# Kernel tuning notes

Measured on AMD Instinct MI355X. Metric: run time of the kernel, lower is better.

Reference implementation:

```python
import jax, jax.numpy as jnp
import numpy as np
from jax import lax

B, T = 2048, 256
V, E, H = 128, 128, 64
POS_WEIGHT = 20.0


def setup_inputs() -> dict:
    key = jax.random.key(0)
    ks = jax.random.split(key, 9)
    # indices in [1, V) so padding_idx=0 row (zeroed) is unused
    x = jax.random.randint(ks[0], (B, T), 1, V)
    targets = (jax.random.uniform(ks[1], (B,)) < 0.05).astype(jnp.float32)
    emb = jax.random.normal(ks[2], (V, E), dtype=jnp.float32).at[0].set(0.0)  # padding_idx=0
    k = 1.0 / np.sqrt(H)
    W_ih = jax.random.uniform(ks[3], (4 * H, E), minval=-k, maxval=k, dtype=jnp.float32)
    W_hh = jax.random.uniform(ks[4], (4 * H, H), minval=-k, maxval=k, dtype=jnp.float32)
    b_ih = jax.random.uniform(ks[5], (4 * H,), minval=-k, maxval=k, dtype=jnp.float32)
    b_hh = jax.random.uniform(ks[6], (4 * H,), minval=-k, maxval=k, dtype=jnp.float32)
    W_fc = jax.random.uniform(ks[7], (1, H), minval=-k, maxval=k, dtype=jnp.float32)
    b_fc = jax.random.uniform(ks[8], (1,), minval=-k, maxval=k, dtype=jnp.float32)
    return {"x": x, "targets": targets, "emb": emb, "W_ih": W_ih, "W_hh": W_hh,
            "b_ih": b_ih, "b_hh": b_hh, "W_fc": W_fc, "b_fc": b_fc}


def reference(x, targets, emb, W_ih, W_hh, b_ih, b_hh, W_fc, b_fc):
    xe = emb[x]  # [B, T, E]
    # precompute input-to-hidden projections for all timesteps: [B, T, 4H]
    xp = jnp.einsum('bte,ge->btg', xe, W_ih) + b_ih + b_hh
    h0 = jnp.zeros((xe.shape[0], W_hh.shape[1]), dtype=xe.dtype)
    c0 = jnp.zeros_like(h0)

    def step(carry, xt):
        h, c = carry
        gates = xt + h @ W_hh.T  # [B, 4H], PyTorch gate order: i, f, g, o
        i, f, g, o = jnp.split(gates, 4, axis=-1)
        c = jax.nn.sigmoid(f) * c + jax.nn.sigmoid(i) * jnp.tanh(g)
        h = jax.nn.sigmoid(o) * jnp.tanh(c)
        return (h, c), None

    (hT, _), _ = lax.scan(step, (h0, c0), jnp.swapaxes(xp, 0, 1))  # scan over time
    logits = (hT @ W_fc.T + b_fc)[:, 0]  # [B]
    # BCEWithLogits with pos_weight, mean reduction (numerically stable)
    loss = -(POS_WEIGHT * targets * jax.nn.log_sigmoid(logits)
             + (1.0 - targets) * jax.nn.log_sigmoid(-logits)).mean()
    return logits, loss
```

## Files before the change

### kernel.cpp

```cpp
#include <hip/hip_runtime.h>
#include <stdint.h>

#define B_ 2048
#define T_ 256
#define V_ 128
#define E_ 128
#define H_ 64
#define G4_ 256
#define POS_W 20.0f
#define MB_ 8
#define NBLK_ (B_ / MB_)

typedef _Float16 half1;
typedef __attribute__((ext_vector_type(8))) _Float16 f16x8;
typedef __attribute__((ext_vector_type(4))) float f32x4;

#if __has_builtin(__builtin_amdgcn_exp2f)
#define EXP2F(x) __builtin_amdgcn_exp2f(x)
#else
#define EXP2F(x) exp2f(x)
#endif

#if __has_builtin(__builtin_amdgcn_rcpf)
#define RCPF(x) __builtin_amdgcn_rcpf(x)
#else
#define RCPF(x) (1.0f / (x))
#endif

__device__ __forceinline__ float sigm(float x) {
    return RCPF(1.0f + EXP2F(-1.44269504f * x));
}
__device__ __forceinline__ float tanhr(float x) {
    float t = EXP2F(2.88539008f * x);
    return 1.0f - 2.0f * RCPF(t + 1.0f);
}

__device__ __forceinline__ void lds_barrier() {
    asm volatile("s_waitcnt lgkmcnt(0)\n\ts_barrier" ::: "memory");
}

__global__ void k_prep(const float* __restrict__ emb, const float* __restrict__ Wih,
                       const float* __restrict__ bih, const float* __restrict__ bhh,
                       float* __restrict__ projC, float* __restrict__ loss_slot) {
    int tid = threadIdx.x;
    int v = blockIdx.x;
    if (v == 0 && tid == 0) *loss_slot = 0.0f;
    int u = tid >> 2, g = tid & 3;
    int row = g * 64 + u;
    const float4* e4 = (const float4*)(emb + v * E_);
    const float4* w4 = (const float4*)(Wih + row * E_);
    float acc = bih[row] + bhh[row];
#pragma unroll
    for (int i = 0; i < E_ / 4; ++i) {
        float4 a = e4[i];
        float4 b = w4[i];
        acc += a.x * b.x + a.y * b.y + a.z * b.z + a.w * b.w;
    }
    projC[v * G4_ + tid] = acc;
}

__launch_bounds__(256, 1)
__global__ void k_lstm(const int* __restrict__ x, const float* __restrict__ Whh,
                       const float* __restrict__ projC, const float* __restrict__ Wfc,
                       const float* __restrict__ bfc, const float* __restrict__ targets,
                       float* __restrict__ logits, float* __restrict__ loss_slot) {
    int b0 = blockIdx.x * MB_;
    int t = threadIdx.x;
    int w = t >> 6, l = t & 63;
    int q = l >> 4, cc = l & 15;
    int u = 16 * w + cc;
    int rA = 2 * q;

    __shared__ __align__(16) half1 hf[2][1024];
    __shared__ int xT[T_][8];
    __shared__ float hfin[MB_][68];
    __shared__ float zred[MB_];

#pragma unroll
    for (int i = 0; i < MB_; ++i) xT[t][i] = x[(b0 + i) * T_ + t];
    ((float*)hf)[t] = 0.0f;
    ((float*)hf)[t + 256] = 0.0f;
    ((float*)hf)[t + 512] = 0.0f;
    ((float*)hf)[t + 768] = 0.0f;
    __syncthreads();

    f16x8 bf[4][2];
#pragma unroll
    for (int jj = 0; jj < 4; ++jj) {
#pragma unroll
        for (int c = 0; c < 2; ++c) {
            int row = jj * 64 + 16 * w + cc;
            int kb = c * 32 + q * 8;
            float4 w0 = *(const float4*)(Whh + row * H_ + kb);
            float4 w1 = *(const float4*)(Whh + row * H_ + kb + 4);
            f16x8 tmp;
            tmp[0] = (half1)w0.x; tmp[1] = (half1)w0.y;
            tmp[2] = (half1)w0.z; tmp[3] = (half1)w0.w;
            tmp[4] = (half1)w1.x; tmp[5] = (half1)w1.y;
            tmp[6] = (half1)w1.z; tmp[7] = (half1)w1.w;
            bf[jj][c] = tmp;
        }
    }

    int hbase = (u >> 5) * 512 + ((u >> 3) & 3) * 128 + (u & 7) + (4 * q) * 8;

    float cA = 0.0f, cB = 0.0f, hA = 0.0f, hB = 0.0f;

    int2 v0 = *(const int2*)&xT[0][rA];
    int2 v1 = *(const int2*)&xT[1][rA];
    f32x4 ppA = *(const f32x4*)(projC + v0.x * G4_ + u * 4);
    f32x4 ppB = *(const f32x4*)(projC + v0.y * G4_ + u * 4);
    f32x4 pnA = *(const f32x4*)(projC + v1.x * G4_ + u * 4);
    f32x4 pnB = *(const f32x4*)(projC + v1.y * G4_ + u * 4);

    int p = 0;
#pragma unroll 2
    for (int step = 0; step < T_; ++step) {
        int2 v2 = *(const int2*)&xT[(step + 2) & (T_ - 1)][rA];
        f32x4 p2A = *(const f32x4*)(projC + v2.x * G4_ + u * 4);
        f32x4 p2B = *(const f32x4*)(projC + v2.y * G4_ + u * 4);

        const f16x8 a0 = *(const f16x8*)(hf[p] + l * 8);
        const f16x8 a1 = *(const f16x8*)(hf[p] + 512 + l * 8);

        f32x4 z4 = {0.0f, 0.0f, 0.0f, 0.0f};
        float gA[4], gB[4];
#pragma unroll
        for (int jj = 0; jj < 4; ++jj) {
            f32x4 d0 = __builtin_amdgcn_mfma_f32_16x16x32_f16(a0, bf[jj][0], z4, 0, 0, 0);
            f32x4 d1 = __builtin_amdgcn_mfma_f32_16x16x32_f16(a1, bf[jj][1], z4, 0, 0, 0);
            gA[jj] = d0[0] + d1[0];
            gB[jj] = d0[1] + d1[1];
        }

        float iA = sigm(gA[0] + ppA.x);
        float fA = sigm(gA[1] + ppA.y);
        float ggA = tanhr(gA[2] + ppA.z);
        float oA = sigm(gA[3] + ppA.w);
        cA = fA * cA + iA * ggA;
        hA = oA * tanhr(cA);

        float iB = sigm(gB[0] + ppB.x);
        float fB = sigm(gB[1] + ppB.y);
        float ggB = tanhr(gB[2] + ppB.z);
        float oB = sigm(gB[3] + ppB.w);
        cB = fB * cB + iB * ggB;
        hB = oB * tanhr(cB);

        half1* hw = hf[p ^ 1] + hbase;
        hw[0] = (half1)hA;
        hw[8] = (half1)hB;

        ppA = pnA; ppB = pnB;
        pnA = p2A; pnB = p2B;
        p ^= 1;
        lds_barrier();
    }

    hfin[rA][u] = hA;
    hfin[rA + 1][u] = hB;
    __syncthreads();
    int m8 = t >> 5, uu = t & 31;
    float part = hfin[m8][2 * uu] * Wfc[2 * uu] + hfin[m8][2 * uu + 1] * Wfc[2 * uu + 1];
#pragma unroll
    for (int off = 16; off > 0; off >>= 1) part += __shfl_down(part, off, 32);
    if (uu == 0) {
        float z = part + bfc[0];
        logits[b0 + m8] = z;
        float tg = targets[b0 + m8];
        float e = EXP2F(-1.44269504f * fabsf(z));
        float lsp = fminf(z, 0.0f) - log1pf(e);
        float lsn = lsp - z;
        zred[m8] = -(POS_W * tg * lsp + (1.0f - tg) * lsn) * (1.0f / (float)B_);
    }
    __syncthreads();
    if (t == 0) {
        float s = 0.0f;
#pragma unroll
        for (int i = 0; i < MB_; ++i) s += zred[i];
        atomicAdd(loss_slot, s);
    }
}

extern "C" void kernel_launch(void* const* d_in, const int* in_sizes, int n_in,
                              void* d_out, int out_size, void* d_ws, size_t ws_size,
                              hipStream_t stream) {
    const int* x = (const int*)d_in[0];
    const float* targets = (const float*)d_in[1];
    const float* emb = (const float*)d_in[2];
    const float* Wih = (const float*)d_in[3];
    const float* Whh = (const float*)d_in[4];
    const float* bih = (const float*)d_in[5];
    const float* bhh = (const float*)d_in[6];
    const float* Wfc = (const float*)d_in[7];
    const float* bfc = (const float*)d_in[8];
    float* out = (float*)d_out;

    float* projC = (float*)d_ws;

    k_prep<<<dim3(V_), dim3(256), 0, stream>>>(emb, Wih, bih, bhh, projC, out + B_);
    k_lstm<<<dim3(NBLK_), dim3(256), 0, stream>>>(x, Whh, projC, Wfc, bfc, targets, out,
                                                  out + B_);
}
```

Measured before the change: 172.2 us.

## Halve batch rows per LSTM block and run two blocks per CU

```diff
diff --git a/kernel.cpp b/kernel.cpp
--- a/kernel.cpp
+++ b/kernel.cpp
@@ -8,9 +8,8 @@
 #define H_ 64
 #define G4_ 256
 #define POS_W 20.0f
-#define MB_ 8
+#define MB_ 4
 #define NBLK_ (B_ / MB_)
-
 typedef _Float16 half1;
 typedef __attribute__((ext_vector_type(8))) _Float16 f16x8;
 typedef __attribute__((ext_vector_type(4))) float f32x4;
@@ -59,7 +58,7 @@
     projC[v * G4_ + tid] = acc;
 }
 
-__launch_bounds__(256, 1)
+__launch_bounds__(256, 2)
 __global__ void k_lstm(const int* __restrict__ x, const float* __restrict__ Whh,
                        const float* __restrict__ projC, const float* __restrict__ Wfc,
                        const float* __restrict__ bfc, const float* __restrict__ targets,
@@ -69,10 +68,9 @@
     int w = t >> 6, l = t & 63;
     int q = l >> 4, cc = l & 15;
     int u = 16 * w + cc;
-    int rA = 2 * q;
 
     __shared__ __align__(16) half1 hf[2][1024];
-    __shared__ int xT[T_][8];
+    __shared__ int xT[T_][MB_];
     __shared__ float hfin[MB_][68];
     __shared__ float zred[MB_];
 
@@ -102,35 +100,28 @@
         }
     }
 
-    int hbase = (u >> 5) * 512 + ((u >> 3) & 3) * 128 + (u & 7) + (4 * q) * 8;
+    int hbase = (u >> 5) * 512 + ((u >> 3) & 3) * 128 + (4 * q) * 8 + (u & 7);
 
-    float cA = 0.0f, cB = 0.0f, hA = 0.0f, hB = 0.0f;
+    float cA = 0.0f, hA = 0.0f;
 
-    int2 v0 = *(const int2*)&xT[0][rA];
-    int2 v1 = *(const int2*)&xT[1][rA];
-    f32x4 ppA = *(const f32x4*)(projC + v0.x * G4_ + u * 4);
-    f32x4 ppB = *(const f32x4*)(projC + v0.y * G4_ + u * 4);
-    f32x4 pnA = *(const f32x4*)(projC + v1.x * G4_ + u * 4);
-    f32x4 pnB = *(const f32x4*)(projC + v1.y * G4_ + u * 4);
+    f32x4 ppA = *(const f32x4*)(projC + xT[0][q] * G4_ + u * 4);
+    f32x4 pnA = *(const f32x4*)(projC + xT[1][q] * G4_ + u * 4);
 
     int p = 0;
 #pragma unroll 2
     for (int step = 0; step < T_; ++step) {
-        int2 v2 = *(const int2*)&xT[(step + 2) & (T_ - 1)][rA];
-        f32x4 p2A = *(const f32x4*)(projC + v2.x * G4_ + u * 4);
-        f32x4 p2B = *(const f32x4*)(projC + v2.y * G4_ + u * 4);
+        f32x4 p2A = *(const f32x4*)(projC + xT[(step + 2) & (T_ - 1)][q] * G4_ + u * 4);
 
         const f16x8 a0 = *(const f16x8*)(hf[p] + l * 8);
         const f16x8 a1 = *(const f16x8*)(hf[p] + 512 + l * 8);
 
         f32x4 z4 = {0.0f, 0.0f, 0.0f, 0.0f};
-        float gA[4], gB[4];
+        float gA[4];
 #pragma unroll
         for (int jj = 0; jj < 4; ++jj) {
             f32x4 d0 = __builtin_amdgcn_mfma_f32_16x16x32_f16(a0, bf[jj][0], z4, 0, 0, 0);
             f32x4 d1 = __builtin_amdgcn_mfma_f32_16x16x32_f16(a1, bf[jj][1], z4, 0, 0, 0);
             gA[jj] = d0[0] + d1[0];
-            gB[jj] = d0[1] + d1[1];
         }
 
         float iA = sigm(gA[0] + ppA.x);
@@ -140,38 +131,28 @@
         cA = fA * cA + iA * ggA;
         hA = oA * tanhr(cA);
 
-        float iB = sigm(gB[0] + ppB.x);
-        float fB = sigm(gB[1] + ppB.y);
-        float ggB = tanhr(gB[2] + ppB.z);
-        float oB = sigm(gB[3] + ppB.w);
-        cB = fB * cB + iB * ggB;
-        hB = oB * tanhr(cB);
+        hf[p ^ 1][hbase] = (half1)hA;
 
-        half1* hw = hf[p ^ 1] + hbase;
-        hw[0] = (half1)hA;
-        hw[8] = (half1)hB;
-
-        ppA = pnA; ppB = pnB;
-        pnA = p2A; pnB = p2B;
+        ppA = pnA;
+        pnA = p2A;
         p ^= 1;
         lds_barrier();
     }
 
-    hfin[rA][u] = hA;
-    hfin[rA + 1][u] = hB;
+    hfin[q][u] = hA;
     __syncthreads();
-    int m8 = t >> 5, uu = t & 31;
-    float part = hfin[m8][2 * uu] * Wfc[2 * uu] + hfin[m8][2 * uu + 1] * Wfc[2 * uu + 1];
+    int m4 = t >> 6, uu = t & 63;
+    float part = hfin[m4][uu] * Wfc[uu];
 #pragma unroll
-    for (int off = 16; off > 0; off >>= 1) part += __shfl_down(part, off, 32);
+    for (int off = 32; off > 0; off >>= 1) part += __shfl_down(part, off, 64);
     if (uu == 0) {
         float z = part + bfc[0];
-        logits[b0 + m8] = z;
-        float tg = targets[b0 + m8];
+        logits[b0 + m4] = z;
+        float tg = targets[b0 + m4];
         float e = EXP2F(-1.44269504f * fabsf(z));
         float lsp = fminf(z, 0.0f) - log1pf(e);
         float lsn = lsp - z;
-        zred[m8] = -(POS_W * tg * lsp + (1.0f - tg) * lsn) * (1.0f / (float)B_);
+        zred[m4] = -(POS_W * tg * lsp + (1.0f - tg) * lsn) * (1.0f / (float)B_);
     }
     __syncthreads();
     if (t == 0) {
```

Result: faster. 163.5 us (-5.0%).
